# Kernel tuning notes

Hardware: AMD Instinct MI355X
Metric: run time of the kernel (lower is better)

## Reference

```python
import jax, jax.numpy as jnp
import numpy as np

B, V, H, K = 65536, 128, 128, 10
L1_REG, L2_REG = 0.0, 1e-4


def setup_inputs() -> dict:
    key = jax.random.key(0)
    ks = jax.random.split(key, 6)
    batch = (jax.random.uniform(ks[0], (B, V)) < 0.5).astype(jnp.float32)  # binary spins
    weights_amp = jax.random.normal(ks[1], (H, V), jnp.float32) / np.sqrt(V).astype(np.float32)
    weights_phase = jax.random.normal(ks[2], (H, V), jnp.float32) / np.sqrt(V).astype(np.float32)
    visible_bias_amp = jnp.zeros((V,), jnp.float32)
    hidden_bias_amp = jnp.zeros((H,), jnp.float32)
    visible_bias_phase = jnp.zeros((V,), jnp.float32)
    hidden_bias_phase = jnp.zeros((H,), jnp.float32)
    noise_h = jax.random.uniform(ks[3], (K, B, H), jnp.float32)  # Bernoulli thresholds for hidden samples
    noise_v = jax.random.uniform(ks[4], (K, B, V), jnp.float32)  # Bernoulli thresholds for visible samples
    return dict(batch=batch, weights_amp=weights_amp, visible_bias_amp=visible_bias_amp,
                hidden_bias_amp=hidden_bias_amp, weights_phase=weights_phase,
                visible_bias_phase=visible_bias_phase, hidden_bias_phase=hidden_bias_phase,
                noise_h=noise_h, noise_v=noise_v)


def reference(batch, weights_amp, visible_bias_amp, hidden_bias_amp,
              weights_phase, visible_bias_phase, hidden_bias_phase,
              noise_h, noise_v):
    bs = batch.shape[0]
    # Positive (data) phase: batched version of the per-sample torch.ger loop (Z-basis path).
    ph0 = jax.nn.sigmoid(batch @ weights_amp.T + hidden_bias_amp)           # [B,H]
    g_w_amp = -(ph0.T @ batch) / bs                                          # [H,V] == -mean outer(ph0, v0)
    g_vb_amp = -jnp.mean(batch, axis=0)
    g_hb_amp = -jnp.mean(ph0, axis=0)

    # CD-k Gibbs sampling on the amplitude RBM, vectorized over the batch.
    def step(v, noise):
        nh, nv = noise
        h = (nh < jax.nn.sigmoid(v @ weights_amp.T + hidden_bias_amp)).astype(v.dtype)
        v_new = (nv < jax.nn.sigmoid(h @ weights_amp + visible_bias_amp)).astype(v.dtype)
        return v_new, None

    vk, _ = jax.lax.scan(step, batch, (noise_h, noise_v))                    # [B,V]

    # Negative (model) phase.
    phk = jax.nn.sigmoid(vk @ weights_amp.T + hidden_bias_amp)               # [B,H]
    g_w_amp = g_w_amp + (phk.T @ vk) / bs
    g_vb_amp = g_vb_amp + jnp.mean(vk, axis=0)
    g_hb_amp = g_hb_amp + jnp.mean(phk, axis=0)

    # Weight regularization (L1 + L2), applied to both amp and phase weight gradients.
    g_w_amp = g_w_amp + L2_REG * weights_amp + L1_REG * jnp.sign(weights_amp)
    g_w_phase = L2_REG * weights_phase + L1_REG * jnp.sign(weights_phase)    # phase grads are zero in Z basis
    g_vb_phase = jnp.zeros_like(visible_bias_phase)
    g_hb_phase = jnp.zeros_like(hidden_bias_phase)

    return (g_w_amp, g_vb_amp, g_hb_amp, g_w_phase, g_vb_phase, g_hb_phase)
```

## Files before the change

### kernel.cpp

```cpp
#include <hip/hip_runtime.h>

typedef float  f32x4 __attribute__((ext_vector_type(4)));
typedef short  s16x8 __attribute__((ext_vector_type(8)));
typedef unsigned int u32x2 __attribute__((ext_vector_type(2)));
typedef unsigned int u32x4 __attribute__((ext_vector_type(4)));

#define NB     65536
#define RPB    256
#define CR     32
#define NCH    8
#define NBLK   256
#define NTHR   512
#define NSTEP  10
#define L2R    1e-4f
#define INVB   (1.0f/65536.0f)

#define OFF_W1H  0
#define OFF_W1L  32768
#define OFF_W2H  65536
#define OFF_W2L  98304
#define OFF_VT   131072
#define OFF_X    139264
#define OFF_VTT  151552
#define OFF_HB   161792
#define OFF_VB   162304
#define SMEM_SZ  162816

__device__ __forceinline__ unsigned short f2bf(float f){
  unsigned int u = __float_as_uint(f);
  u += 0x7fffu + ((u>>16)&1u);
  return (unsigned short)(u>>16);
}
__device__ __forceinline__ float bf2f(unsigned short s){
  return __uint_as_float(((unsigned int)s)<<16);
}
__device__ __forceinline__ float sigm(float x){
  return __fdividef(1.0f, 1.0f + __expf(-x));
}
__device__ __forceinline__ int swz(int row, int byteInRow){
  return (row<<8) + (byteInRow ^ ((row&7)<<4));
}
__device__ __forceinline__ u32x2 pack4(unsigned short a, unsigned short b,
                                       unsigned short c, unsigned short d){
  u32x2 r; r[0] = (unsigned int)a | ((unsigned int)b<<16);
  r[1] = (unsigned int)c | ((unsigned int)d<<16); return r;
}

__device__ __forceinline__ void matvec128(const char* Ahi, const char* Alo, const char* Bb,
                                          int lane, int w, f32x4& c0, f32x4& c1){
  const int arow = (w<<4) + (lane&15);
  const int br0  = lane&15;
  const int br1  = 16 + (lane&15);
  const int koff = (lane>>4)<<4;
  c0 = (f32x4){0.f,0.f,0.f,0.f};
  c1 = (f32x4){0.f,0.f,0.f,0.f};
  #pragma unroll
  for(int kk=0;kk<4;kk++){
    const int bIR = (kk<<6) + koff;
    s16x8 ah = *(const s16x8*)(Ahi + swz(arow,bIR));
    s16x8 al = *(const s16x8*)(Alo + swz(arow,bIR));
    s16x8 b0 = *(const s16x8*)(Bb  + swz(br0 ,bIR));
    s16x8 b1 = *(const s16x8*)(Bb  + swz(br1 ,bIR));
    c0 = __builtin_amdgcn_mfma_f32_16x16x32_bf16(ah,b0,c0,0,0,0);
    c0 = __builtin_amdgcn_mfma_f32_16x16x32_bf16(al,b0,c0,0,0,0);
    c1 = __builtin_amdgcn_mfma_f32_16x16x32_bf16(ah,b1,c1,0,0,0);
    c1 = __builtin_amdgcn_mfma_f32_16x16x32_bf16(al,b1,c1,0,0,0);
  }
}

extern "C" __global__ void __launch_bounds__(NTHR)
rbm_main(const float* __restrict__ batch,
         const float* __restrict__ wamp,
         const float* __restrict__ vbias,
         const float* __restrict__ hbias,
         const float* __restrict__ nh_g,
         const float* __restrict__ nv_g,
         float* __restrict__ out)
{
  extern __shared__ char smem[];
  char* W1H = smem+OFF_W1H;  char* W1L = smem+OFF_W1L;
  char* W2H = smem+OFF_W2H;  char* W2L = smem+OFF_W2L;
  char* VT  = smem+OFF_VT;   char* X   = smem+OFF_X;
  char* VTT = smem+OFF_VTT;
  float* hbL = (float*)(smem+OFF_HB);
  float* vbL = (float*)(smem+OFF_VB);

  const int t    = threadIdx.x;
  const int lane = t & 63;
  const int w    = t >> 6;

  {
    const int j    = t>>2;
    const int iseg = (t&3)<<5;
    const float* src = wamp + j*128 + iseg;
    #pragma unroll
    for(int g=0; g<4; g++){
      f32x4 a0 = *(const f32x4*)(src + (g<<3));
      f32x4 a1 = *(const f32x4*)(src + (g<<3) + 4);
      float vv[8] = {a0[0],a0[1],a0[2],a0[3],a1[0],a1[1],a1[2],a1[3]};
      unsigned short hi[8], lo[8];
      #pragma unroll
      for(int e=0;e<8;e++){
        unsigned short h = f2bf(vv[e]);
        hi[e]=h; lo[e]=f2bf(vv[e] - bf2f(h));
      }
      u32x4 ph_, pl_;
      ph_[0]=hi[0]|((unsigned)hi[1]<<16); ph_[1]=hi[2]|((unsigned)hi[3]<<16);
      ph_[2]=hi[4]|((unsigned)hi[5]<<16); ph_[3]=hi[6]|((unsigned)hi[7]<<16);
      pl_[0]=lo[0]|((unsigned)lo[1]<<16); pl_[1]=lo[2]|((unsigned)lo[3]<<16);
      pl_[2]=lo[4]|((unsigned)lo[5]<<16); pl_[3]=lo[6]|((unsigned)lo[7]<<16);
      const int cbyte = (iseg + (g<<3))<<1;
      *(u32x4*)(W1H + swz(j, cbyte)) = ph_;
      *(u32x4*)(W1L + swz(j, cbyte)) = pl_;
      #pragma unroll
      for(int e=0;e<8;e++){
        const int i = iseg+(g<<3)+e;
        *(unsigned short*)(W2H + swz(i, j<<1)) = hi[e];
        *(unsigned short*)(W2L + swz(i, j<<1)) = lo[e];
      }
    }
    if(t<128){ hbL[t]=hbias[t]; vbL[t]=vbias[t]; }
  }

  f32x4 S[8];
  #pragma unroll
  for(int n=0;n<8;n++) S[n]=(f32x4){0.f,0.f,0.f,0.f};
  float hbacc[4]={0,0,0,0};
  float vbs[8]={0,0,0,0,0,0,0,0};
  float vbl[8]={0,0,0,0,0,0,0,0};

  __syncthreads();

  const int j0 = (w<<4) + ((lane>>4)<<2);
  const f32x4 hbv = *(const f32x4*)(hbL + j0);
  const f32x4 vbv = *(const f32x4*)(vbL + j0);
  const long blkrow = (long)blockIdx.x * RPB;

  for(int ch=0; ch<NCH; ch++){
    const int r0 = (int)blkrow + ch*CR;

    {
      const int lr = t>>4;
      const int cb = (t&15)<<3;
      const float* src = batch + ((long)(r0+lr)<<7) + cb;
      f32x4 a0 = *(const f32x4*)(src);
      f32x4 a1 = *(const f32x4*)(src+4);
      float vv[8] = {a0[0],a0[1],a0[2],a0[3],a1[0],a1[1],a1[2],a1[3]};
      unsigned short bb[8];
      #pragma unroll
      for(int e=0;e<8;e++){ bb[e]=f2bf(vv[e]); vbl[e]-=vv[e]; }
      u32x4 pw;
      pw[0]=bb[0]|((unsigned)bb[1]<<16); pw[1]=bb[2]|((unsigned)bb[3]<<16);
      pw[2]=bb[4]|((unsigned)bb[5]<<16); pw[3]=bb[6]|((unsigned)bb[7]<<16);
      *(u32x4*)(VT + swz(lr, cb<<1)) = pw;
      #pragma unroll
      for(int e=0;e<8;e++)
        *(unsigned short*)(VTT + (cb+e)*80 + (lr<<1)) = bb[e];
    }
    __syncthreads();

    const int R0 = r0 + (lane&15);
    const int R1 = R0 + 16;

    f32x4 nh0 = *(const f32x4*)(nh_g + ((long)R0<<7) + j0);
    f32x4 nh1 = *(const f32x4*)(nh_g + ((long)R1<<7) + j0);
    f32x4 nv0 = *(const f32x4*)(nv_g + ((long)R0<<7) + j0);
    f32x4 nv1 = *(const f32x4*)(nv_g + ((long)R1<<7) + j0);

    f32x4 c0,c1;
    matvec128(W1H,W1L,VT,lane,w,c0,c1);
    float p0[4],p1[4];
    #pragma unroll
    for(int r2=0;r2<4;r2++){
      p0[r2]=sigm(c0[r2]+hbv[r2]);
      p1[r2]=sigm(c1[r2]+hbv[r2]);
      hbacc[r2]-=p0[r2]+p1[r2];
      *(unsigned short*)(X + (j0+r2)*80 + ((lane&15)<<1))      = f2bf(-p0[r2]);
      *(unsigned short*)(X + (j0+r2)*80 + ((16+(lane&15))<<1)) = f2bf(-p1[r2]);
    }
    __syncthreads();
    {
      const int arow = (w<<4)+(lane&15);
      const int koff = (lane>>4)<<4;
      s16x8 a = *(const s16x8*)(X + arow*80 + koff);
      #pragma unroll
      for(int n=0;n<8;n++){
        s16x8 b = *(const s16x8*)(VTT + ((n<<4)+(lane&15))*80 + koff);
        S[n] = __builtin_amdgcn_mfma_f32_16x16x32_bf16(a,b,S[n],0,0,0);
      }
    }
    __syncthreads();
    *(u32x2*)(X + swz(lane&15, j0<<1)) =
      pack4(nh0[0]<p0[0]?0x3f80:0, nh0[1]<p0[1]?0x3f80:0,
            nh0[2]<p0[2]?0x3f80:0, nh0[3]<p0[3]?0x3f80:0);
    *(u32x2*)(X + swz(16+(lane&15), j0<<1)) =
      pack4(nh1[0]<p1[0]?0x3f80:0, nh1[1]<p1[1]?0x3f80:0,
            nh1[2]<p1[2]?0x3f80:0, nh1[3]<p1[3]?0x3f80:0);
    __syncthreads();

    for(int k=0;k<NSTEP;k++){
      const bool pf = (k<NSTEP-1);
      const long kb = (long)(k+1)*NB;
      if(pf){
        nh0 = *(const f32x4*)(nh_g + ((kb+R0)<<7) + j0);
        nh1 = *(const f32x4*)(nh_g + ((kb+R1)<<7) + j0);
      }
      matvec128(W2H,W2L,X,lane,w,c0,c1);
      unsigned short q0[4],q1[4];
      float vn0[4],vn1[4];
      #pragma unroll
      for(int r2=0;r2<4;r2++){
        float s0=sigm(c0[r2]+vbv[r2]);
        float s1=sigm(c1[r2]+vbv[r2]);
        vn0[r2]=(nv0[r2]<s0)?1.0f:0.0f;  q0[r2]=(nv0[r2]<s0)?0x3f80:0;
        vn1[r2]=(nv1[r2]<s1)?1.0f:0.0f;  q1[r2]=(nv1[r2]<s1)?0x3f80:0;
      }
      *(u32x2*)(VT + swz(lane&15,      j0<<1)) = pack4(q0[0],q0[1],q0[2],q0[3]);
      *(u32x2*)(VT + swz(16+(lane&15), j0<<1)) = pack4(q1[0],q1[1],q1[2],q1[3]);
      if(k==NSTEP-1){
        #pragma unroll
        for(int r2=0;r2<4;r2++){
          *(unsigned short*)(VTT + (j0+r2)*80 + ((lane&15)<<1))      = q0[r2];
          *(unsigned short*)(VTT + (j0+r2)*80 + ((16+(lane&15))<<1)) = q1[r2];
          vbs[r2]+=vn0[r2]; vbs[4+r2]+=vn1[r2];
        }
      }
      __syncthreads();
      if(pf){
        nv0 = *(const f32x4*)(nv_g + ((kb+R0)<<7) + j0);
        nv1 = *(const f32x4*)(nv_g + ((kb+R1)<<7) + j0);
        matvec128(W1H,W1L,VT,lane,w,c0,c1);
        #pragma unroll
        for(int r2=0;r2<4;r2++){
          float s0=sigm(c0[r2]+hbv[r2]);
          float s1=sigm(c1[r2]+hbv[r2]);
          q0[r2]=(nh0[r2]<s0)?0x3f80:0;
          q1[r2]=(nh1[r2]<s1)?0x3f80:0;
        }
        *(u32x2*)(X + swz(lane&15,      j0<<1)) = pack4(q0[0],q0[1],q0[2],q0[3]);
        *(u32x2*)(X + swz(16+(lane&15), j0<<1)) = pack4(q1[0],q1[1],q1[2],q1[3]);
        __syncthreads();
      }
    }

    matvec128(W1H,W1L,VT,lane,w,c0,c1);
    #pragma unroll
    for(int r2=0;r2<4;r2++){
      p0[r2]=sigm(c0[r2]+hbv[r2]);
      p1[r2]=sigm(c1[r2]+hbv[r2]);
      hbacc[r2]+=p0[r2]+p1[r2];
      *(unsigned short*)(X + (j0+r2)*80 + ((lane&15)<<1))      = f2bf(p0[r2]);
      *(unsigned short*)(X + (j0+r2)*80 + ((16+(lane&15))<<1)) = f2bf(p1[r2]);
    }
    __syncthreads();
    {
      const int arow = (w<<4)+(lane&15);
      const int koff = (lane>>4)<<4;
      s16x8 a = *(const s16x8*)(X + arow*80 + koff);
      #pragma unroll
      for(int n=0;n<8;n++){
        s16x8 b = *(const s16x8*)(VTT + ((n<<4)+(lane&15))*80 + koff);
        S[n] = __builtin_amdgcn_mfma_f32_16x16x32_bf16(a,b,S[n],0,0,0);
      }
    }
    __syncthreads();
  }

  #pragma unroll
  for(int n=0;n<8;n++){
    #pragma unroll
    for(int r2=0;r2<4;r2++){
      const int e = ((w<<4)+((lane>>4)<<2)+r2)*128 + (n<<4)+(lane&15);
      atomicAdd(out + e, S[n][r2]*INVB);
    }
  }
  if(t<128){ hbL[t]=0.f; vbL[t]=0.f; }
  __syncthreads();
  #pragma unroll
  for(int r2=0;r2<4;r2++){
    atomicAdd(&hbL[j0+r2], hbacc[r2]);
    atomicAdd(&vbL[j0+r2], vbs[r2]+vbs[4+r2]);
  }
  {
    const int cb=(t&15)<<3;
    #pragma unroll
    for(int e=0;e<8;e++) atomicAdd(&vbL[cb+e], vbl[e]);
  }
  __syncthreads();
  if(t<128){
    atomicAdd(out+16384+t, vbL[t]*INVB);
    atomicAdd(out+16512+t, hbL[t]*INVB);
  }
}

extern "C" __global__ void __launch_bounds__(256)
rbm_finalize(const float* __restrict__ wamp, const float* __restrict__ wphase,
             float* __restrict__ out)
{
  const int tid = blockIdx.x*256 + threadIdx.x;
  if(tid < 16384){
    out[tid]       += L2R * wamp[tid];
    out[16640+tid]  = L2R * wphase[tid];
  } else if(tid < 16640){
    out[16640+tid]  = 0.0f;
  }
}

extern "C" void kernel_launch(void* const* d_in, const int* in_sizes, int n_in,
                              void* d_out, int out_size, void* d_ws, size_t ws_size,
                              hipStream_t stream) {
  (void)in_sizes; (void)n_in; (void)d_ws; (void)ws_size; (void)out_size;
  const float* batch  = (const float*)d_in[0];
  const float* wamp   = (const float*)d_in[1];
  const float* vbias  = (const float*)d_in[2];
  const float* hbias  = (const float*)d_in[3];
  const float* wphase = (const float*)d_in[4];
  const float* nh     = (const float*)d_in[7];
  const float* nv     = (const float*)d_in[8];
  float* out = (float*)d_out;

  hipFuncSetAttribute((const void*)rbm_main,
                      hipFuncAttributeMaxDynamicSharedMemorySize, SMEM_SZ);

  hipMemsetAsync(d_out, 0, (size_t)33280*sizeof(float), stream);
  rbm_main<<<dim3(NBLK), dim3(NTHR), SMEM_SZ, stream>>>(batch, wamp, vbias, hbias, nh, nv, out);
  rbm_finalize<<<dim3(65), dim3(256), 0, stream>>>(wamp, wphase, out);
}
```

Before: 726.7 us.

## Hold weight fragments in registers, drop sigmoid divide, reduce via workspace

Loads all bf16 hi/lo weight fragments for both matvec directions into registers once, so LDS reads of weights inside the Gibbs loop go away. Sampling now compares nv*(1+exp(-x)) < 1 instead of computing the sigmoid with a divide. The transposed copy of the visible chunk is built from the swizzled layout instead of with scattered stores. When the workspace is large enough, per-block partial gradients go to it and a separate reduce kernel sums them, replacing global float atomics and the memset. The cost is much higher register pressure under launch_bounds(512,2), plus an extra pass over the workspace in the reduce kernel.

New measurement: 698.6 us. 1.04x faster.

```diff
diff --git a/kernel.cpp b/kernel.cpp
--- a/kernel.cpp
+++ b/kernel.cpp
@@ -6,6 +6,7 @@
 typedef unsigned int u32x4 __attribute__((ext_vector_type(4)));
 
 #define NB     65536
+#define NBH    (65536*128)
 #define RPB    256
 #define CR     32
 #define NCH    8
@@ -14,6 +15,8 @@
 #define NSTEP  10
 #define L2R    1e-4f
 #define INVB   (1.0f/65536.0f)
+#define WSPB   16640
+#define WS_NEED ((size_t)NBLK*WSPB*sizeof(float))
 
 #define OFF_W1H  0
 #define OFF_W1L  32768
@@ -46,40 +49,35 @@
   r[1] = (unsigned int)c | ((unsigned int)d<<16); return r;
 }
 
-__device__ __forceinline__ void matvec128(const char* Ahi, const char* Alo, const char* Bb,
-                                          int lane, int w, f32x4& c0, f32x4& c1){
-  const int arow = (w<<4) + (lane&15);
-  const int br0  = lane&15;
-  const int br1  = 16 + (lane&15);
-  const int koff = (lane>>4)<<4;
-  c0 = (f32x4){0.f,0.f,0.f,0.f};
-  c1 = (f32x4){0.f,0.f,0.f,0.f};
-  #pragma unroll
-  for(int kk=0;kk<4;kk++){
-    const int bIR = (kk<<6) + koff;
-    s16x8 ah = *(const s16x8*)(Ahi + swz(arow,bIR));
-    s16x8 al = *(const s16x8*)(Alo + swz(arow,bIR));
-    s16x8 b0 = *(const s16x8*)(Bb  + swz(br0 ,bIR));
-    s16x8 b1 = *(const s16x8*)(Bb  + swz(br1 ,bIR));
-    c0 = __builtin_amdgcn_mfma_f32_16x16x32_bf16(ah,b0,c0,0,0,0);
-    c0 = __builtin_amdgcn_mfma_f32_16x16x32_bf16(al,b0,c0,0,0,0);
-    c1 = __builtin_amdgcn_mfma_f32_16x16x32_bf16(ah,b1,c1,0,0,0);
-    c1 = __builtin_amdgcn_mfma_f32_16x16x32_bf16(al,b1,c1,0,0,0);
-  }
-}
-
-extern "C" __global__ void __launch_bounds__(NTHR)
-rbm_main(const float* __restrict__ batch,
+#define MF(a,b,c) __builtin_amdgcn_mfma_f32_16x16x32_bf16(a,b,c,0,0,0)
+#define MATVEC(H0,H1,H2,H3,L0,L1,L2,L3,B0,B1,B2,B3)                      \
+  do{ s16x8 b0_,b1_;                                                     \
+    c0=(f32x4){0.f,0.f,0.f,0.f}; c1=(f32x4){0.f,0.f,0.f,0.f};           \
+    b0_=*(const s16x8*)(B0); b1_=*(const s16x8*)((B0)+4096);             \
+    c0=MF(H0,b0_,c0); c0=MF(L0,b0_,c0); c1=MF(H0,b1_,c1); c1=MF(L0,b1_,c1);\
+    b0_=*(const s16x8*)(B1); b1_=*(const s16x8*)((B1)+4096);             \
+    c0=MF(H1,b0_,c0); c0=MF(L1,b0_,c0); c1=MF(H1,b1_,c1); c1=MF(L1,b1_,c1);\
+    b0_=*(const s16x8*)(B2); b1_=*(const s16x8*)((B2)+4096);             \
+    c0=MF(H2,b0_,c0); c0=MF(L2,b0_,c0); c1=MF(H2,b1_,c1); c1=MF(L2,b1_,c1);\
+    b0_=*(const s16x8*)(B3); b1_=*(const s16x8*)((B3)+4096);             \
+    c0=MF(H3,b0_,c0); c0=MF(L3,b0_,c0); c1=MF(H3,b1_,c1); c1=MF(L3,b1_,c1);\
+  }while(0)
+#define MATVEC_H() MATVEC(W1H0,W1H1,W1H2,W1H3,W1L0,W1L1,W1L2,W1L3,bVT0,bVT1,bVT2,bVT3)
+#define MATVEC_V() MATVEC(W2H0,W2H1,W2H2,W2H3,W2L0,W2L1,W2L2,W2L3,bX0,bX1,bX2,bX3)
+
+template<bool USE_WS>
+__global__ __launch_bounds__(NTHR, 2) void rbm_main_t(
+         const float* __restrict__ batch,
          const float* __restrict__ wamp,
          const float* __restrict__ vbias,
          const float* __restrict__ hbias,
          const float* __restrict__ nh_g,
          const float* __restrict__ nv_g,
-         float* __restrict__ out)
+         float* __restrict__ sink)
 {
   extern __shared__ char smem[];
-  char* W1H = smem+OFF_W1H;  char* W1L = smem+OFF_W1L;
-  char* W2H = smem+OFF_W2H;  char* W2L = smem+OFF_W2L;
+  char* W1Hp = smem+OFF_W1H;  char* W1Lp = smem+OFF_W1L;
+  char* W2Hp = smem+OFF_W2H;  char* W2Lp = smem+OFF_W2L;
   char* VT  = smem+OFF_VT;   char* X   = smem+OFF_X;
   char* VTT = smem+OFF_VTT;
   float* hbL = (float*)(smem+OFF_HB);
@@ -110,17 +108,50 @@
       pl_[0]=lo[0]|((unsigned)lo[1]<<16); pl_[1]=lo[2]|((unsigned)lo[3]<<16);
       pl_[2]=lo[4]|((unsigned)lo[5]<<16); pl_[3]=lo[6]|((unsigned)lo[7]<<16);
       const int cbyte = (iseg + (g<<3))<<1;
-      *(u32x4*)(W1H + swz(j, cbyte)) = ph_;
-      *(u32x4*)(W1L + swz(j, cbyte)) = pl_;
+      *(u32x4*)(W1Hp + swz(j, cbyte)) = ph_;
+      *(u32x4*)(W1Lp + swz(j, cbyte)) = pl_;
       #pragma unroll
       for(int e=0;e<8;e++){
         const int i = iseg+(g<<3)+e;
-        *(unsigned short*)(W2H + swz(i, j<<1)) = hi[e];
-        *(unsigned short*)(W2L + swz(i, j<<1)) = lo[e];
+        *(unsigned short*)(W2Hp + swz(i, j<<1)) = hi[e];
+        *(unsigned short*)(W2Lp + swz(i, j<<1)) = lo[e];
       }
     }
     if(t<128){ hbL[t]=hbias[t]; vbL[t]=vbias[t]; }
   }
+  __syncthreads();
+
+  const int r15  = lane&15;
+  const int koff = (lane>>4)<<4;
+  const int j0   = (w<<4) + ((lane>>4)<<2);
+  s16x8 W1H0,W1H1,W1H2,W1H3, W1L0,W1L1,W1L2,W1L3;
+  s16x8 W2H0,W2H1,W2H2,W2H3, W2L0,W2L1,W2L2,W2L3;
+  {
+    const int ar = (w<<4) + r15;
+    W1H0=*(const s16x8*)(W1Hp+swz(ar,  0+koff)); W1L0=*(const s16x8*)(W1Lp+swz(ar,  0+koff));
+    W1H1=*(const s16x8*)(W1Hp+swz(ar, 64+koff)); W1L1=*(const s16x8*)(W1Lp+swz(ar, 64+koff));
+    W1H2=*(const s16x8*)(W1Hp+swz(ar,128+koff)); W1L2=*(const s16x8*)(W1Lp+swz(ar,128+koff));
+    W1H3=*(const s16x8*)(W1Hp+swz(ar,192+koff)); W1L3=*(const s16x8*)(W1Lp+swz(ar,192+koff));
+    W2H0=*(const s16x8*)(W2Hp+swz(ar,  0+koff)); W2L0=*(const s16x8*)(W2Lp+swz(ar,  0+koff));
+    W2H1=*(const s16x8*)(W2Hp+swz(ar, 64+koff)); W2L1=*(const s16x8*)(W2Lp+swz(ar, 64+koff));
+    W2H2=*(const s16x8*)(W2Hp+swz(ar,128+koff)); W2L2=*(const s16x8*)(W2Lp+swz(ar,128+koff));
+    W2H3=*(const s16x8*)(W2Hp+swz(ar,192+koff)); W2L3=*(const s16x8*)(W2Lp+swz(ar,192+koff));
+  }
+
+  char* aVT = VT + swz(r15, j0<<1);
+  char* aX  = X  + swz(r15, j0<<1);
+  const char* bVT0 = VT + swz(r15,   0+koff);
+  const char* bVT1 = VT + swz(r15,  64+koff);
+  const char* bVT2 = VT + swz(r15, 128+koff);
+  const char* bVT3 = VT + swz(r15, 192+koff);
+  const char* bX0  = X  + swz(r15,   0+koff);
+  const char* bX1  = X  + swz(r15,  64+koff);
+  const char* bX2  = X  + swz(r15, 128+koff);
+  const char* bX3  = X  + swz(r15, 192+koff);
+  const char* vttA = VTT + r15*80 + koff;
+  const char* phA  = X   + ((w<<4)+r15)*80 + koff;
+  char* vtW = VTT + j0*80 + (r15<<1);
+  char* phW = X   + j0*80 + (r15<<1);
 
   f32x4 S[8];
   #pragma unroll
@@ -129,9 +160,6 @@
   float vbs[8]={0,0,0,0,0,0,0,0};
   float vbl[8]={0,0,0,0,0,0,0,0};
 
-  __syncthreads();
-
-  const int j0 = (w<<4) + ((lane>>4)<<2);
   const f32x4 hbv = *(const f32x4*)(hbL + j0);
   const f32x4 vbv = *(const f32x4*)(vbL + j0);
   const long blkrow = (long)blockIdx.x * RPB;
@@ -153,143 +181,195 @@
       pw[0]=bb[0]|((unsigned)bb[1]<<16); pw[1]=bb[2]|((unsigned)bb[3]<<16);
       pw[2]=bb[4]|((unsigned)bb[5]<<16); pw[3]=bb[6]|((unsigned)bb[7]<<16);
       *(u32x4*)(VT + swz(lr, cb<<1)) = pw;
-      #pragma unroll
-      for(int e=0;e<8;e++)
-        *(unsigned short*)(VTT + (cb+e)*80 + (lr<<1)) = bb[e];
-    }
-    __syncthreads();
-
-    const int R0 = r0 + (lane&15);
-    const int R1 = R0 + 16;
-
-    f32x4 nh0 = *(const f32x4*)(nh_g + ((long)R0<<7) + j0);
-    f32x4 nh1 = *(const f32x4*)(nh_g + ((long)R1<<7) + j0);
-    f32x4 nv0 = *(const f32x4*)(nv_g + ((long)R0<<7) + j0);
-    f32x4 nv1 = *(const f32x4*)(nv_g + ((long)R1<<7) + j0);
+    }
+    __syncthreads();
+
+    const int R0 = r0 + r15;
+    const float* nb_h0 = nh_g + ((long)R0<<7) + j0;
+    const float* nb_h1 = nb_h0 + (16<<7);
+    const float* nb_v0 = nv_g + ((long)R0<<7) + j0;
+    const float* nb_v1 = nb_v0 + (16<<7);
+    f32x4 nh0 = *(const f32x4*)nb_h0;
+    f32x4 nh1 = *(const f32x4*)nb_h1;
+    f32x4 nv0 = *(const f32x4*)nb_v0;
+    f32x4 nv1 = *(const f32x4*)nb_v1;
+    const float* pnh0 = nb_h0 + NBH;  const float* pnh1 = nb_h1 + NBH;
+    const float* pnv0 = nb_v0 + NBH;  const float* pnv1 = nb_v1 + NBH;
+
+    {
+      u32x2 a0 = *(const u32x2*)(aVT);
+      u32x2 a1 = *(const u32x2*)(aVT+4096);
+      *(unsigned short*)(vtW +   0) = (unsigned short)(a0[0]);
+      *(unsigned short*)(vtW +  80) = (unsigned short)(a0[0]>>16);
+      *(unsigned short*)(vtW + 160) = (unsigned short)(a0[1]);
+      *(unsigned short*)(vtW + 240) = (unsigned short)(a0[1]>>16);
+      *(unsigned short*)(vtW +  32) = (unsigned short)(a1[0]);
+      *(unsigned short*)(vtW + 112) = (unsigned short)(a1[0]>>16);
+      *(unsigned short*)(vtW + 192) = (unsigned short)(a1[1]);
+      *(unsigned short*)(vtW + 272) = (unsigned short)(a1[1]>>16);
+    }
 
     f32x4 c0,c1;
-    matvec128(W1H,W1L,VT,lane,w,c0,c1);
+    MATVEC_H();
     float p0[4],p1[4];
     #pragma unroll
     for(int r2=0;r2<4;r2++){
       p0[r2]=sigm(c0[r2]+hbv[r2]);
       p1[r2]=sigm(c1[r2]+hbv[r2]);
       hbacc[r2]-=p0[r2]+p1[r2];
-      *(unsigned short*)(X + (j0+r2)*80 + ((lane&15)<<1))      = f2bf(-p0[r2]);
-      *(unsigned short*)(X + (j0+r2)*80 + ((16+(lane&15))<<1)) = f2bf(-p1[r2]);
-    }
-    __syncthreads();
-    {
-      const int arow = (w<<4)+(lane&15);
-      const int koff = (lane>>4)<<4;
-      s16x8 a = *(const s16x8*)(X + arow*80 + koff);
+      *(unsigned short*)(phW + r2*80)      = f2bf(-p0[r2]);
+      *(unsigned short*)(phW + r2*80 + 32) = f2bf(-p1[r2]);
+    }
+    __syncthreads();
+    {
+      s16x8 a = *(const s16x8*)(phA);
       #pragma unroll
       for(int n=0;n<8;n++){
-        s16x8 b = *(const s16x8*)(VTT + ((n<<4)+(lane&15))*80 + koff);
-        S[n] = __builtin_amdgcn_mfma_f32_16x16x32_bf16(a,b,S[n],0,0,0);
-      }
-    }
-    __syncthreads();
-    *(u32x2*)(X + swz(lane&15, j0<<1)) =
-      pack4(nh0[0]<p0[0]?0x3f80:0, nh0[1]<p0[1]?0x3f80:0,
-            nh0[2]<p0[2]?0x3f80:0, nh0[3]<p0[3]?0x3f80:0);
-    *(u32x2*)(X + swz(16+(lane&15), j0<<1)) =
-      pack4(nh1[0]<p1[0]?0x3f80:0, nh1[1]<p1[1]?0x3f80:0,
-            nh1[2]<p1[2]?0x3f80:0, nh1[3]<p1[3]?0x3f80:0);
+        s16x8 b = *(const s16x8*)(vttA + n*1280);
+        S[n] = MF(a,b,S[n]);
+      }
+    }
+    __syncthreads();
+    *(u32x2*)(aX)      = pack4(nh0[0]<p0[0]?0x3f80:0, nh0[1]<p0[1]?0x3f80:0,
+                               nh0[2]<p0[2]?0x3f80:0, nh0[3]<p0[3]?0x3f80:0);
+    *(u32x2*)(aX+4096) = pack4(nh1[0]<p1[0]?0x3f80:0, nh1[1]<p1[1]?0x3f80:0,
+                               nh1[2]<p1[2]?0x3f80:0, nh1[3]<p1[3]?0x3f80:0);
     __syncthreads();
 
     for(int k=0;k<NSTEP;k++){
       const bool pf = (k<NSTEP-1);
-      const long kb = (long)(k+1)*NB;
       if(pf){
-        nh0 = *(const f32x4*)(nh_g + ((kb+R0)<<7) + j0);
-        nh1 = *(const f32x4*)(nh_g + ((kb+R1)<<7) + j0);
-      }
-      matvec128(W2H,W2L,X,lane,w,c0,c1);
+        nh0 = *(const f32x4*)pnh0;  pnh0 += NBH;
+        nh1 = *(const f32x4*)pnh1;  pnh1 += NBH;
+      }
+      MATVEC_V();
       unsigned short q0[4],q1[4];
-      float vn0[4],vn1[4];
       #pragma unroll
       for(int r2=0;r2<4;r2++){
-        float s0=sigm(c0[r2]+vbv[r2]);
-        float s1=sigm(c1[r2]+vbv[r2]);
-        vn0[r2]=(nv0[r2]<s0)?1.0f:0.0f;  q0[r2]=(nv0[r2]<s0)?0x3f80:0;
-        vn1[r2]=(nv1[r2]<s1)?1.0f:0.0f;  q1[r2]=(nv1[r2]<s1)?0x3f80:0;
-      }
-      *(u32x2*)(VT + swz(lane&15,      j0<<1)) = pack4(q0[0],q0[1],q0[2],q0[3]);
-      *(u32x2*)(VT + swz(16+(lane&15), j0<<1)) = pack4(q1[0],q1[1],q1[2],q1[3]);
+        float E0 = __expf(-(c0[r2]+vbv[r2]));
+        float E1 = __expf(-(c1[r2]+vbv[r2]));
+        q0[r2] = (__fmaf_rn(nv0[r2],E0,nv0[r2]) < 1.0f) ? 0x3f80 : 0;
+        q1[r2] = (__fmaf_rn(nv1[r2],E1,nv1[r2]) < 1.0f) ? 0x3f80 : 0;
+      }
+      *(u32x2*)(aVT)      = pack4(q0[0],q0[1],q0[2],q0[3]);
+      *(u32x2*)(aVT+4096) = pack4(q1[0],q1[1],q1[2],q1[3]);
       if(k==NSTEP-1){
         #pragma unroll
         for(int r2=0;r2<4;r2++){
-          *(unsigned short*)(VTT + (j0+r2)*80 + ((lane&15)<<1))      = q0[r2];
-          *(unsigned short*)(VTT + (j0+r2)*80 + ((16+(lane&15))<<1)) = q1[r2];
-          vbs[r2]+=vn0[r2]; vbs[4+r2]+=vn1[r2];
+          *(unsigned short*)(vtW + r2*80)      = q0[r2];
+          *(unsigned short*)(vtW + r2*80 + 32) = q1[r2];
+          vbs[r2]   += q0[r2] ? 1.0f : 0.0f;
+          vbs[4+r2] += q1[r2] ? 1.0f : 0.0f;
         }
       }
       __syncthreads();
       if(pf){
-        nv0 = *(const f32x4*)(nv_g + ((kb+R0)<<7) + j0);
-        nv1 = *(const f32x4*)(nv_g + ((kb+R1)<<7) + j0);
-        matvec128(W1H,W1L,VT,lane,w,c0,c1);
+        nv0 = *(const f32x4*)pnv0;  pnv0 += NBH;
+        nv1 = *(const f32x4*)pnv1;  pnv1 += NBH;
+        MATVEC_H();
         #pragma unroll
         for(int r2=0;r2<4;r2++){
-          float s0=sigm(c0[r2]+hbv[r2]);
-          float s1=sigm(c1[r2]+hbv[r2]);
-          q0[r2]=(nh0[r2]<s0)?0x3f80:0;
-          q1[r2]=(nh1[r2]<s1)?0x3f80:0;
+          float E0 = __expf(-(c0[r2]+hbv[r2]));
+          float E1 = __expf(-(c1[r2]+hbv[r2]));
+          q0[r2] = (__fmaf_rn(nh0[r2],E0,nh0[r2]) < 1.0f) ? 0x3f80 : 0;
+          q1[r2] = (__fmaf_rn(nh1[r2],E1,nh1[r2]) < 1.0f) ? 0x3f80 : 0;
         }
-        *(u32x2*)(X + swz(lane&15,      j0<<1)) = pack4(q0[0],q0[1],q0[2],q0[3]);
-        *(u32x2*)(X + swz(16+(lane&15), j0<<1)) = pack4(q1[0],q1[1],q1[2],q1[3]);
+        *(u32x2*)(aX)      = pack4(q0[0],q0[1],q0[2],q0[3]);
+        *(u32x2*)(aX+4096) = pack4(q1[0],q1[1],q1[2],q1[3]);
         __syncthreads();
       }
     }
 
-    matvec128(W1H,W1L,VT,lane,w,c0,c1);
+    MATVEC_H();
     #pragma unroll
     for(int r2=0;r2<4;r2++){
       p0[r2]=sigm(c0[r2]+hbv[r2]);
       p1[r2]=sigm(c1[r2]+hbv[r2]);
       hbacc[r2]+=p0[r2]+p1[r2];
-      *(unsigned short*)(X + (j0+r2)*80 + ((lane&15)<<1))      = f2bf(p0[r2]);
-      *(unsigned short*)(X + (j0+r2)*80 + ((16+(lane&15))<<1)) = f2bf(p1[r2]);
-    }
-    __syncthreads();
-    {
-      const int arow = (w<<4)+(lane&15);
-      const int koff = (lane>>4)<<4;
-      s16x8 a = *(const s16x8*)(X + arow*80 + koff);
+      *(unsigned short*)(phW + r2*80)      = f2bf(p0[r2]);
+      *(unsigned short*)(phW + r2*80 + 32) = f2bf(p1[r2]);
+    }
+    __syncthreads();
+    {
+      s16x8 a = *(const s16x8*)(phA);
       #pragma unroll
       for(int n=0;n<8;n++){
-        s16x8 b = *(const s16x8*)(VTT + ((n<<4)+(lane&15))*80 + koff);
-        S[n] = __builtin_amdgcn_mfma_f32_16x16x32_bf16(a,b,S[n],0,0,0);
-      }
-    }
-    __syncthreads();
-  }
-
-  #pragma unroll
-  for(int n=0;n<8;n++){
+        s16x8 b = *(const s16x8*)(vttA + n*1280);
+        S[n] = MF(a,b,S[n]);
+      }
+    }
+    __syncthreads();
+  }
+
+  if(USE_WS){
+    float* wsb = sink + (long)blockIdx.x*WSPB;
+    #pragma unroll
+    for(int n=0;n<8;n++){
+      #pragma unroll
+      for(int r2=0;r2<4;r2++)
+        wsb[(j0+r2)*128 + (n<<4) + r15] = S[n][r2];
+    }
+    if(t<128){ hbL[t]=0.f; vbL[t]=0.f; }
+    __syncthreads();
     #pragma unroll
     for(int r2=0;r2<4;r2++){
-      const int e = ((w<<4)+((lane>>4)<<2)+r2)*128 + (n<<4)+(lane&15);
-      atomicAdd(out + e, S[n][r2]*INVB);
-    }
-  }
-  if(t<128){ hbL[t]=0.f; vbL[t]=0.f; }
-  __syncthreads();
-  #pragma unroll
-  for(int r2=0;r2<4;r2++){
-    atomicAdd(&hbL[j0+r2], hbacc[r2]);
-    atomicAdd(&vbL[j0+r2], vbs[r2]+vbs[4+r2]);
-  }
-  {
-    const int cb=(t&15)<<3;
-    #pragma unroll
-    for(int e=0;e<8;e++) atomicAdd(&vbL[cb+e], vbl[e]);
-  }
-  __syncthreads();
-  if(t<128){
-    atomicAdd(out+16384+t, vbL[t]*INVB);
-    atomicAdd(out+16512+t, hbL[t]*INVB);
+      atomicAdd(&hbL[j0+r2], hbacc[r2]);
+      atomicAdd(&vbL[j0+r2], vbs[r2]+vbs[4+r2]);
+    }
+    {
+      const int cb=(t&15)<<3;
+      #pragma unroll
+      for(int e=0;e<8;e++) atomicAdd(&vbL[cb+e], vbl[e]);
+    }
+    __syncthreads();
+    if(t<128){
+      wsb[16384+t] = vbL[t];
+      wsb[16512+t] = hbL[t];
+    }
+  } else {
+    float* out = sink;
+    #pragma unroll
+    for(int n=0;n<8;n++){
+      #pragma unroll
+      for(int r2=0;r2<4;r2++)
+        atomicAdd(out + (j0+r2)*128 + (n<<4)+r15, S[n][r2]*INVB);
+    }
+    if(t<128){ hbL[t]=0.f; vbL[t]=0.f; }
+    __syncthreads();
+    #pragma unroll
+    for(int r2=0;r2<4;r2++){
+      atomicAdd(&hbL[j0+r2], hbacc[r2]);
+      atomicAdd(&vbL[j0+r2], vbs[r2]+vbs[4+r2]);
+    }
+    {
+      const int cb=(t&15)<<3;
+      #pragma unroll
+      for(int e=0;e<8;e++) atomicAdd(&vbL[cb+e], vbl[e]);
+    }
+    __syncthreads();
+    if(t<128){
+      atomicAdd(out+16384+t, vbL[t]*INVB);
+      atomicAdd(out+16512+t, hbL[t]*INVB);
+    }
+  }
+}
+
+extern "C" __global__ void __launch_bounds__(256)
+rbm_reduce(const float* __restrict__ ws, const float* __restrict__ wamp,
+           const float* __restrict__ wphase, float* __restrict__ out)
+{
+  const int tid = blockIdx.x*256 + threadIdx.x;
+  if(tid < 16640){
+    float s = 0.f;
+    const float* p = ws + tid;
+    #pragma unroll 4
+    for(int b=0;b<NBLK;b++) s += p[(long)b*WSPB];
+    if(tid<16384) out[tid] = s*INVB + L2R*wamp[tid];
+    else          out[tid] = s*INVB;
+  } else if(tid < 33024){
+    out[tid] = L2R * wphase[tid-16640];
+  } else if(tid < 33280){
+    out[tid] = 0.0f;
   }
 }
 
@@ -309,7 +389,7 @@
 extern "C" void kernel_launch(void* const* d_in, const int* in_sizes, int n_in,
                               void* d_out, int out_size, void* d_ws, size_t ws_size,
                               hipStream_t stream) {
-  (void)in_sizes; (void)n_in; (void)d_ws; (void)ws_size; (void)out_size;
+  (void)in_sizes; (void)n_in; (void)out_size;
   const float* batch  = (const float*)d_in[0];
   const float* wamp   = (const float*)d_in[1];
   const float* vbias  = (const float*)d_in[2];
@@ -319,10 +399,18 @@
   const float* nv     = (const float*)d_in[8];
   float* out = (float*)d_out;
 
-  hipFuncSetAttribute((const void*)rbm_main,
-                      hipFuncAttributeMaxDynamicSharedMemorySize, SMEM_SZ);
-
-  hipMemsetAsync(d_out, 0, (size_t)33280*sizeof(float), stream);
-  rbm_main<<<dim3(NBLK), dim3(NTHR), SMEM_SZ, stream>>>(batch, wamp, vbias, hbias, nh, nv, out);
-  rbm_finalize<<<dim3(65), dim3(256), 0, stream>>>(wamp, wphase, out);
-}
+  if(ws_size >= WS_NEED){
+    hipFuncSetAttribute(reinterpret_cast<const void*>(&rbm_main_t<true>),
+                        hipFuncAttributeMaxDynamicSharedMemorySize, SMEM_SZ);
+    rbm_main_t<true><<<dim3(NBLK), dim3(NTHR), SMEM_SZ, stream>>>(
+        batch, wamp, vbias, hbias, nh, nv, (float*)d_ws);
+    rbm_reduce<<<dim3(130), dim3(256), 0, stream>>>((const float*)d_ws, wamp, wphase, out);
+  } else {
+    hipFuncSetAttribute(reinterpret_cast<const void*>(&rbm_main_t<false>),
+                        hipFuncAttributeMaxDynamicSharedMemorySize, SMEM_SZ);
+    hipMemsetAsync(d_out, 0, (size_t)33280*sizeof(float), stream);
+    rbm_main_t<false><<<dim3(NBLK), dim3(NTHR), SMEM_SZ, stream>>>(
+        batch, wamp, vbias, hbias, nh, nv, out);
+    rbm_finalize<<<dim3(65), dim3(256), 0, stream>>>(wamp, wphase, out);
+  }
+}
```
